# Performance work log

Hardware: AMD Instinct MI355X
Metric: run time of the kernel (lower is better)

The kernel has to match this reference:

```python
import jax, jax.numpy as jnp
import numpy as np
import math

B, C, S, O, K = 64, 271, 512, 512, 32  # seq_len S must equal out_channels O (einsum constraint in original)

def setup_inputs() -> dict:
    key = jax.random.key(0)
    k1, k2, k3, k4, k5 = jax.random.split(key, 5)
    x = jax.random.normal(k1, (B, C, S), dtype=jnp.float32)
    fourier_features = jax.random.normal(k2, (O, K, K, 4), dtype=jnp.float32)
    sensor_positions = jax.random.uniform(k3, (C, 2), dtype=jnp.float32)
    proj_w = jax.random.normal(k4, (O, C), dtype=jnp.float32) / np.float32(math.sqrt(C))
    proj_b = jax.random.normal(k5, (O,), dtype=jnp.float32) * 0.02
    return {"x": x, "fourier_features": fourier_features,
            "sensor_positions": sensor_positions, "proj_w": proj_w, "proj_b": proj_b}

def reference(x, fourier_features, sensor_positions, proj_w, proj_b):
    Kdim = fourier_features.shape[1]
    freqs = 2.0 * jnp.pi * jnp.arange(Kdim, dtype=jnp.float32) / Kdim
    # meshgrid(freqs_x, freqs_y, indexing='ij') stacked on last dim -> [K,K,2]
    grid = jnp.stack(jnp.meshgrid(freqs, freqs, indexing='ij'), axis=-1)
    # feature map is batch-independent: [C,K,K,2] -> sin/cos cat -> [C,K,K,4]
    fm = sensor_positions[:, None, None, :] * grid[None]
    fm = jnp.concatenate([jnp.sin(fm), jnp.cos(fm)], axis=-1)
    # attention logits [O,C]; original expands over batch but result is identical per batch
    att = jnp.einsum('ckhw,okhw->oc', fm, fourier_features)
    att = jax.nn.softmax(att, axis=0)  # softmax over out_channels (dim=1 of [B,O,C])
    # 1x1 Conv1d: [B,C,S] -> [B,O,S]
    xp = jnp.einsum('bcs,oc->bos', x, proj_w) + proj_b[None, :, None]
    # original: einsum('bci,bio->bco', xp[B,O,S], attn[B,O,C]); contraction over S(==O)
    out = jnp.einsum('bps,sq->bpq', xp, att)  # [B,O,C]
    return out
```

## Files before the change

### kernel.cpp

```cpp
#include <hip/hip_runtime.h>
#include <hip/hip_bf16.h>
#include <math.h>


typedef short s16x8 __attribute__((ext_vector_type(8)));
typedef short s16x4 __attribute__((ext_vector_type(4)));
typedef float f32x4 __attribute__((ext_vector_type(4)));

#define GLOBAL_AS __attribute__((address_space(1)))
#define LDS_AS    __attribute__((address_space(3)))

__device__ __forceinline__ short f2bf(float f) {
    __hip_bfloat16 h = __float2bfloat16(f);
    return *reinterpret_cast<short*>(&h);
}

#define Cdim 271
#define CpK  288
#define Sdim 512
#define Odim 512
#define MF   17344
#define MFp  17408

template<int MODE, int SWAP>
__global__ __launch_bounds__(512, 6) void gemm_bf16(
    const short* __restrict__ A, int lda,
    const short* __restrict__ BT, int ldb,
    int nk,
    void* __restrict__ OutV,
    const float* __restrict__ bias)
{
    const int m0 = (SWAP ? blockIdx.x : blockIdx.y) * 128;
    const int n0 = (SWAP ? blockIdx.y : blockIdx.x) * 128;

    __shared__ short pool[24576];

    const int t = threadIdx.x;
    const int lane = t & 63;
    const int wid = t >> 6;
    const int wr = wid >> 2;
    const int wc = wid & 3;
    const int lr = lane & 15, lkq = lane >> 4;

    f32x4 acc[4][2];
    #pragma unroll
    for (int i = 0; i < 4; ++i)
        #pragma unroll
        for (int j = 0; j < 2; ++j)
            acc[i][j] = (f32x4){0.f, 0.f, 0.f, 0.f};

    const int srow = wid * 16 + (lane >> 2);
    const int skk  = (((lane & 3) ^ ((lane >> 3) & 3)) * 8);
    const short* pA = A + (long)(m0 + srow) * lda + skk;
    const short* pB = BT + (long)(n0 + srow) * ldb + skk;
    const int ldsOff = wid * 512;

    const int kxs = ((lkq ^ ((lr >> 1) & 3)) << 3);
    const int aBase = (wr * 64 + lr) * 32 + kxs;
    const int bBase = (wc * 32 + lr) * 32 + kxs;

    auto stage = [&](int buf, int kt) {
        const int k0 = kt * 32;
        __builtin_amdgcn_global_load_lds((const GLOBAL_AS void*)(pA + k0),
            (LDS_AS void*)&pool[buf * 4096 + ldsOff], 16, 0, 0);
        __builtin_amdgcn_global_load_lds((const GLOBAL_AS void*)(pB + k0),
            (LDS_AS void*)&pool[12288 + buf * 4096 + ldsOff], 16, 0, 0);
    };

    auto compute = [&](int buf) {
        s16x8 af[4], bfv[2];
        #pragma unroll
        for (int m = 0; m < 4; ++m)
            af[m] = *(const s16x8*)&pool[buf * 4096 + aBase + m * 512];
        #pragma unroll
        for (int n = 0; n < 2; ++n)
            bfv[n] = *(const s16x8*)&pool[12288 + buf * 4096 + bBase + n * 512];
        #pragma unroll
        for (int m = 0; m < 4; ++m)
            #pragma unroll
            for (int n = 0; n < 2; ++n)
                acc[m][n] = __builtin_amdgcn_mfma_f32_16x16x32_bf16(af[m], bfv[n], acc[m][n], 0, 0, 0);
    };

    stage(0, 0); stage(1, 1);
    int bc = 0, bs = 2;
    for (int kt = 0; kt < nk; ++kt) {
        if (kt + 1 < nk) asm volatile("s_waitcnt vmcnt(2)" ::: "memory");
        else             asm volatile("s_waitcnt vmcnt(0)" ::: "memory");
        __builtin_amdgcn_s_barrier();
        __builtin_amdgcn_sched_barrier(0);
        if (kt + 2 < nk) stage(bs, kt + 2);
        compute(bc);
        bc = (bc == 2) ? 0 : bc + 1;
        bs = (bs == 2) ? 0 : bs + 1;
    }

    if (MODE == 0) {
        __syncthreads();
        short* T = pool;
        #pragma unroll
        for (int i = 0; i < 4; ++i) {
            const int ml = wr * 64 + i * 16 + lkq * 4;
            #pragma unroll
            for (int j = 0; j < 2; ++j) {
                const int ql = wc * 32 + j * 16 + lr;
                s16x4 v;
                #pragma unroll
                for (int r = 0; r < 4; ++r) v[r] = f2bf(acc[i][j][r]);
                *(s16x4*)&T[ql * 132 + ml] = v;
            }
        }
        __syncthreads();
        short* Oy = (short*)OutV;
        #pragma unroll
        for (int p = 0; p < 4; ++p) {
            const int ql = p * 32 + (t >> 4);
            const int gq = n0 + ql;
            const int mlc = (t & 15) * 8;
            const s16x8 v = *(const s16x8*)&T[ql * 132 + mlc];
            const int gm0 = m0 + mlc;
            if (gq < Cdim && gm0 < MF) {
                const int b0 = gm0 / Cdim;
                const int c0 = gm0 - b0 * Cdim;
                if (c0 + 8 <= Cdim) {
                    *(s16x8*)&Oy[((long)b0 * Cdim + gq) * CpK + c0] = v;
                } else {
                    #pragma unroll
                    for (int r = 0; r < 8; ++r) {
                        const int gm = gm0 + r;
                        if (gm < MF) {
                            const int bb = gm / Cdim;
                            const int cc = gm - bb * Cdim;
                            Oy[((long)bb * Cdim + gq) * CpK + cc] = v[r];
                        }
                    }
                }
            }
        }
    } else {
        float* O = (float*)OutV;
        #pragma unroll
        for (int j = 0; j < 2; ++j) {
            const int gn = n0 + wc * 32 + j * 16 + lr;
            if (gn >= MF) continue;
            const int b = gn / Cdim;
            const int q = gn - b * Cdim;
            float* ob = O + (long)b * Odim * Cdim + q;
            #pragma unroll
            for (int i = 0; i < 4; ++i) {
                const int gmb = m0 + wr * 64 + i * 16 + lkq * 4;
                #pragma unroll
                for (int r = 0; r < 4; ++r) {
                    const int gm = gmb + r;
                    ob[(long)gm * Cdim] = acc[i][j][r] + bias[gm];
                }
            }
        }
    }
}

#define CONVX_BLOCKS 4352
#define PW_BLOCKS    576
#define FF_BLOCKS    256

__global__ __launch_bounds__(256) void prep(
    const float* __restrict__ x,  short* __restrict__ xb,
    const float* __restrict__ pw, short* __restrict__ pwb,
    const float* __restrict__ ff, float* __restrict__ GT)
{
    const int blk = blockIdx.x;
    const int t = threadIdx.x;

    if (blk < CONVX_BLOCKS) {
        const long i8 = ((long)blk * 256 + t) * 8;
        s16x8 v = {0, 0, 0, 0, 0, 0, 0, 0};
        if (i8 < (long)MF * Sdim) {
            const f32x4 u0 = *(const f32x4*)&x[i8];
            const f32x4 u1 = *(const f32x4*)&x[i8 + 4];
            #pragma unroll
            for (int j = 0; j < 4; ++j) { v[j] = f2bf(u0[j]); v[4 + j] = f2bf(u1[j]); }
        }
        *(s16x8*)&xb[i8] = v;
        return;
    }
    if (blk < CONVX_BLOCKS + PW_BLOCKS) {
        const int idx = (blk - CONVX_BLOCKS) * 256 + t;
        const int p = idx / CpK;
        const int k = idx - p * CpK;
        pwb[idx] = (k < Cdim) ? f2bf(pw[(long)p * Cdim + k]) : (short)0;
        return;
    }
    __shared__ float L[2][32 * 132];
    const int fb = blk - (CONVX_BLOCKS + PW_BLOCKS);
    const int half = t >> 7;
    const int tl = t & 127;
    const int o = fb * 2 + half;
    const float* base = ff + (long)o * 4096;
    #pragma unroll
    for (int ch = 0; ch < 8; ++ch) {
        const int g = ch * 512 + tl * 4;
        const f32x4 v = *(const f32x4*)&base[g];
        *(f32x4*)&L[half][(g >> 7) * 132 + (g & 127)] = v;
    }
    __syncthreads();
    const int gq = tl >> 5, idx = tl & 31;
    float s = 0.f;
    if (gq == 0 || gq == 2) {
        const int w = (gq == 0) ? 0 : 2;
        #pragma unroll 8
        for (int j = 0; j < 32; ++j) s += L[half][idx * 132 + j * 4 + w];
    } else {
        const int w = (gq == 1) ? 1 : 3;
        #pragma unroll 8
        for (int i = 0; i < 32; ++i) s += L[half][i * 132 + idx * 4 + w];
    }
    GT[tl * 512 + o] = s;
}

__device__ __forceinline__ float wave_max(float v) {
    #pragma unroll
    for (int off = 32; off; off >>= 1) v = fmaxf(v, __shfl_xor(v, off));
    return v;
}
__device__ __forceinline__ float wave_sum(float v) {
    #pragma unroll
    for (int off = 32; off; off >>= 1) v += __shfl_xor(v, off);
    return v;
}

__global__ __launch_bounds__(256) void att_fused(
    const float* __restrict__ GT,
    const float* __restrict__ sp,
    short* __restrict__ attT)
{
    const int c = blockIdx.x;
    const int t = threadIdx.x;
    short* row = attT + (long)c * Sdim;
    if (c >= Cdim) {
        row[t] = 0; row[t + 256] = 0;
        return;
    }
    __shared__ float u[128];
    __shared__ float red[4];
    if (t < 128) {
        const int g = t >> 5, k = t & 31;
        const float f = 6.283185307179586477f * (float)k / 32.0f;
        const float p = sp[c * 2 + (g & 1)];
        const float ang = p * f;
        u[t] = (g < 2) ? sinf(ang) : cosf(ang);
    }
    __syncthreads();

    float l0 = 0.f, l1 = 0.f;
    #pragma unroll 8
    for (int k = 0; k < 128; ++k) {
        const float uk = u[k];
        l0 = fmaf(GT[k * 512 + t], uk, l0);
        l1 = fmaf(GT[k * 512 + t + 256], uk, l1);
    }

    const int lane = t & 63, wid = t >> 6;
    float m = wave_max(fmaxf(l0, l1));
    if (lane == 0) red[wid] = m;
    __syncthreads();
    m = fmaxf(fmaxf(red[0], red[1]), fmaxf(red[2], red[3]));
    const float e0 = expf(l0 - m), e1 = expf(l1 - m);
    float s = wave_sum(e0 + e1);
    __syncthreads();
    if (lane == 0) red[wid] = s;
    __syncthreads();
    s = red[0] + red[1] + red[2] + red[3];
    const float inv = 1.f / s;
    row[t]       = f2bf(e0 * inv);
    row[t + 256] = f2bf(e1 * inv);
}

extern "C" void kernel_launch(void* const* d_in, const int* in_sizes, int n_in,
                              void* d_out, int out_size, void* d_ws, size_t ws_size,
                              hipStream_t stream)
{
    const float* x  = (const float*)d_in[0];
    const float* ff = (const float*)d_in[1];
    const float* sp = (const float*)d_in[2];
    const float* pw = (const float*)d_in[3];
    const float* pb = (const float*)d_in[4];
    float* out = (float*)d_out;

    const int S = Sdim, O = Odim;

    float* ws   = (float*)d_ws;
    float* GT   = ws;
    short* xb   = (short*)(GT + 128 * 512);
    short* attT = xb + (long)MFp * S;
    short* pwb  = attT + 384L * S;
    short* yT   = pwb + (long)O * CpK;

    prep<<<CONVX_BLOCKS + PW_BLOCKS + FF_BLOCKS, 256, 0, stream>>>(
        x, xb, pw, pwb, ff, GT);

    att_fused<<<384, 256, 0, stream>>>(GT, sp, attT);

    gemm_bf16<0, 1><<<dim3(MFp / 128, 3), 512, 0, stream>>>(
        xb, S, attT, S, S / 32, (void*)yT, nullptr);

    gemm_bf16<1, 0><<<dim3(MFp / 128, O / 128), 512, 0, stream>>>(
        pwb, CpK, yT, CpK, CpK / 32, (void*)out, pb);
}
```

Before: 60.99 us.

## Fuse fp32-to-bf16 conversion of x into first GEMM's A-tile loads

Drops the separate pass that converted all of x to a bf16 workspace. The first GEMM now loads fp32 rows of x into registers, converts them to bf16 and writes them into LDS, with a register-prefetch pipeline one stage ahead. The proj_w conversion moves into spare blocks of the attention kernel and the Fourier reduction becomes its own small kernel. This avoids writing and re-reading about 17 MB of bf16 intermediate, at the cost of fp32 global loads, extra registers and VALU conversion work inside the GEMM main loop. The occupancy hint on the GEMM launch bounds is removed.

```diff
diff --git a/kernel.cpp b/kernel.cpp
--- a/kernel.cpp
+++ b/kernel.cpp
@@ -22,9 +22,9 @@
 #define MF   17344
 #define MFp  17408
 
-template<int MODE, int SWAP>
-__global__ __launch_bounds__(512, 6) void gemm_bf16(
-    const short* __restrict__ A, int lda,
+template<int MODE, int SWAP, int AF32>
+__global__ __launch_bounds__(512) void gemm_bf16(
+    const void* __restrict__ Av, int lda,
     const short* __restrict__ BT, int ldb,
     int nk,
     void* __restrict__ OutV,
@@ -49,22 +49,30 @@
         for (int j = 0; j < 2; ++j)
             acc[i][j] = (f32x4){0.f, 0.f, 0.f, 0.f};
 
-    const int srow = wid * 16 + (lane >> 2);
-    const int skk  = (((lane & 3) ^ ((lane >> 3) & 3)) * 8);
-    const short* pA = A + (long)(m0 + srow) * lda + skk;
-    const short* pB = BT + (long)(n0 + srow) * ldb + skk;
+    const int srowB = wid * 16 + (lane >> 2);
+    const int skk   = (((lane & 3) ^ ((lane >> 3) & 3)) * 8);
+    const short* pB = BT + (long)(n0 + srowB) * ldb + skk;
     const int ldsOff = wid * 512;
+
+    const short* pA_bf = (const short*)Av + (long)(m0 + srowB) * lda + skk;
+    const int arow = t >> 2;
+    const int aslot = t & 3;
+    const int afc = (aslot ^ ((arow >> 1) & 3)) * 8;
+    const int agrow = (m0 + arow < MF) ? (m0 + arow) : (MF - 1);
+    const float* pA_f32 = (const float*)Av + (long)agrow * lda + afc;
+    const int aWr = arow * 32 + aslot * 8;
 
     const int kxs = ((lkq ^ ((lr >> 1) & 3)) << 3);
     const int aBase = (wr * 64 + lr) * 32 + kxs;
     const int bBase = (wc * 32 + lr) * 32 + kxs;
 
-    auto stage = [&](int buf, int kt) {
-        const int k0 = kt * 32;
-        __builtin_amdgcn_global_load_lds((const GLOBAL_AS void*)(pA + k0),
+    auto stageB = [&](int buf, int kt) {
+        __builtin_amdgcn_global_load_lds((const GLOBAL_AS void*)(pB + kt * 32),
+            (LDS_AS void*)&pool[12288 + buf * 4096 + ldsOff], 16, 0, 0);
+    };
+    auto stageA_bf = [&](int buf, int kt) {
+        __builtin_amdgcn_global_load_lds((const GLOBAL_AS void*)(pA_bf + kt * 32),
             (LDS_AS void*)&pool[buf * 4096 + ldsOff], 16, 0, 0);
-        __builtin_amdgcn_global_load_lds((const GLOBAL_AS void*)(pB + k0),
-            (LDS_AS void*)&pool[12288 + buf * 4096 + ldsOff], 16, 0, 0);
     };
 
     auto compute = [&](int buf) {
@@ -82,17 +90,49 @@
                 acc[m][n] = __builtin_amdgcn_mfma_f32_16x16x32_bf16(af[m], bfv[n], acc[m][n], 0, 0, 0);
     };
 
-    stage(0, 0); stage(1, 1);
-    int bc = 0, bs = 2;
-    for (int kt = 0; kt < nk; ++kt) {
-        if (kt + 1 < nk) asm volatile("s_waitcnt vmcnt(2)" ::: "memory");
-        else             asm volatile("s_waitcnt vmcnt(0)" ::: "memory");
-        __builtin_amdgcn_s_barrier();
-        __builtin_amdgcn_sched_barrier(0);
-        if (kt + 2 < nk) stage(bs, kt + 2);
-        compute(bc);
-        bc = (bc == 2) ? 0 : bc + 1;
-        bs = (bs == 2) ? 0 : bs + 1;
+    if (AF32) {
+        f32x4 aP0, aP1, aN0, aN1;
+        auto loadA = [&](int kt, f32x4& v0, f32x4& v1) {
+            const float* p = pA_f32 + kt * 32;
+            v0 = *(const f32x4 GLOBAL_AS*)(p);
+            v1 = *(const f32x4 GLOBAL_AS*)(p + 4);
+        };
+        auto writeA = [&](int buf, const f32x4& v0, const f32x4& v1) {
+            s16x8 w;
+            #pragma unroll
+            for (int j = 0; j < 4; ++j) { w[j] = f2bf(v0[j]); w[4 + j] = f2bf(v1[j]); }
+            *(s16x8*)&pool[buf * 4096 + aWr] = w;
+        };
+        loadA(0, aP0, aP1); stageB(0, 0);
+        writeA(0, aP0, aP1);
+        loadA(1, aP0, aP1); stageB(1, 1);
+        int bc = 0, bs = 2;
+        for (int kt = 0; kt < nk; ++kt) {
+            if (kt + 1 < nk) asm volatile("s_waitcnt vmcnt(3) lgkmcnt(0)" ::: "memory");
+            else             asm volatile("s_waitcnt vmcnt(0) lgkmcnt(0)" ::: "memory");
+            __builtin_amdgcn_s_barrier();
+            __builtin_amdgcn_sched_barrier(0);
+            if (kt + 2 < nk) { loadA(kt + 2, aN0, aN1); stageB(bs, kt + 2); }
+            compute(bc);
+            if (kt + 1 < nk) writeA((bc == 2) ? 0 : bc + 1, aP0, aP1);
+            aP0 = aN0; aP1 = aN1;
+            bc = (bc == 2) ? 0 : bc + 1;
+            bs = (bs == 2) ? 0 : bs + 1;
+        }
+    } else {
+        stageA_bf(0, 0); stageB(0, 0);
+        stageA_bf(1, 1); stageB(1, 1);
+        int bc = 0, bs = 2;
+        for (int kt = 0; kt < nk; ++kt) {
+            if (kt + 1 < nk) asm volatile("s_waitcnt vmcnt(2)" ::: "memory");
+            else             asm volatile("s_waitcnt vmcnt(0)" ::: "memory");
+            __builtin_amdgcn_s_barrier();
+            __builtin_amdgcn_sched_barrier(0);
+            if (kt + 2 < nk) { stageA_bf(bs, kt + 2); stageB(bs, kt + 2); }
+            compute(bc);
+            bc = (bc == 2) ? 0 : bc + 1;
+            bs = (bs == 2) ? 0 : bs + 1;
+        }
     }
 
     if (MODE == 0) {
@@ -159,42 +199,14 @@
     }
 }
 
-#define CONVX_BLOCKS 4352
-#define PW_BLOCKS    576
-#define FF_BLOCKS    256
-
-__global__ __launch_bounds__(256) void prep(
-    const float* __restrict__ x,  short* __restrict__ xb,
-    const float* __restrict__ pw, short* __restrict__ pwb,
-    const float* __restrict__ ff, float* __restrict__ GT)
+__global__ __launch_bounds__(256) void ff_reduce(const float* __restrict__ ff,
+                                                 float* __restrict__ GT)
 {
-    const int blk = blockIdx.x;
+    __shared__ float L[2][32 * 132];
     const int t = threadIdx.x;
-
-    if (blk < CONVX_BLOCKS) {
-        const long i8 = ((long)blk * 256 + t) * 8;
-        s16x8 v = {0, 0, 0, 0, 0, 0, 0, 0};
-        if (i8 < (long)MF * Sdim) {
-            const f32x4 u0 = *(const f32x4*)&x[i8];
-            const f32x4 u1 = *(const f32x4*)&x[i8 + 4];
-            #pragma unroll
-            for (int j = 0; j < 4; ++j) { v[j] = f2bf(u0[j]); v[4 + j] = f2bf(u1[j]); }
-        }
-        *(s16x8*)&xb[i8] = v;
-        return;
-    }
-    if (blk < CONVX_BLOCKS + PW_BLOCKS) {
-        const int idx = (blk - CONVX_BLOCKS) * 256 + t;
-        const int p = idx / CpK;
-        const int k = idx - p * CpK;
-        pwb[idx] = (k < Cdim) ? f2bf(pw[(long)p * Cdim + k]) : (short)0;
-        return;
-    }
-    __shared__ float L[2][32 * 132];
-    const int fb = blk - (CONVX_BLOCKS + PW_BLOCKS);
     const int half = t >> 7;
     const int tl = t & 127;
-    const int o = fb * 2 + half;
+    const int o = blockIdx.x * 2 + half;
     const float* base = ff + (long)o * 4096;
     #pragma unroll
     for (int ch = 0; ch < 8; ++ch) {
@@ -231,13 +243,28 @@
 __global__ __launch_bounds__(256) void att_fused(
     const float* __restrict__ GT,
     const float* __restrict__ sp,
-    short* __restrict__ attT)
+    short* __restrict__ attT,
+    const float* __restrict__ pw,
+    short* __restrict__ pwb)
 {
     const int c = blockIdx.x;
     const int t = threadIdx.x;
     short* row = attT + (long)c * Sdim;
     if (c >= Cdim) {
         row[t] = 0; row[t + 256] = 0;
+        const int bi = c - Cdim;
+        if (bi < 72) {
+            const int idx8 = (bi * 256 + t) * 8;
+            const int p = idx8 / CpK;
+            const int k0 = idx8 - p * CpK;
+            s16x8 v;
+            #pragma unroll
+            for (int r = 0; r < 8; ++r) {
+                const int k = k0 + r;
+                v[r] = (k < Cdim) ? f2bf(pw[(long)p * Cdim + k]) : (short)0;
+            }
+            *(s16x8*)&pwb[idx8] = v;
+        }
         return;
     }
     __shared__ float u[128];
@@ -290,19 +317,17 @@
 
     float* ws   = (float*)d_ws;
     float* GT   = ws;
-    short* xb   = (short*)(GT + 128 * 512);
-    short* attT = xb + (long)MFp * S;
+    short* attT = (short*)(GT + 128 * 512);
     short* pwb  = attT + 384L * S;
     short* yT   = pwb + (long)O * CpK;
 
-    prep<<<CONVX_BLOCKS + PW_BLOCKS + FF_BLOCKS, 256, 0, stream>>>(
-        x, xb, pw, pwb, ff, GT);
-
-    att_fused<<<384, 256, 0, stream>>>(GT, sp, attT);
-
-    gemm_bf16<0, 1><<<dim3(MFp / 128, 3), 512, 0, stream>>>(
-        xb, S, attT, S, S / 32, (void*)yT, nullptr);
-
-    gemm_bf16<1, 0><<<dim3(MFp / 128, O / 128), 512, 0, stream>>>(
-        pwb, CpK, yT, CpK, CpK / 32, (void*)out, pb);
-}
+    ff_reduce<<<256, 256, 0, stream>>>(ff, GT);
+
+    att_fused<<<384, 256, 0, stream>>>(GT, sp, attT, pw, pwb);
+
+    gemm_bf16<0, 1, 1><<<dim3(MFp / 128, 3), 512, 0, stream>>>(
+        (const void*)x, S, attT, S, S / 32, (void*)yT, nullptr);
+
+    gemm_bf16<1, 0, 0><<<dim3(MFp / 128, O / 128), 512, 0, stream>>>(
+        (const void*)pwb, CpK, yT, CpK, CpK / 32, (void*)out, pb);
+}
```

Result: faster. 57.95 us (-5.0%).
